# Kernel tuning notes

Measured on AMD Instinct MI355X. Metric: run time of the kernel, lower is better.

The kernel has to match this reference:

```python
import jax, jax.numpy as jnp
import numpy as np

C_M, C_Z, C, N_HEAD = 256, 128, 32, 8
N_SEQ, N_RES = 256, 256
LN_EPS = 1e-5


def _layer_norm(x, w, b):
    mu = jnp.mean(x, axis=-1, keepdims=True)
    var = jnp.var(x, axis=-1, keepdims=True)
    return (x - mu) * jax.lax.rsqrt(var + LN_EPS) * w + b


def setup_inputs() -> dict:
    key = jax.random.key(0)
    ks = jax.random.split(key, 12)
    s = 0.02
    return {
        "m": jax.random.normal(ks[0], (N_SEQ, N_RES, C_M), dtype=jnp.float32),
        "z": jax.random.normal(ks[1], (N_RES, N_RES, C_Z), dtype=jnp.float32),
        "ln_m_w": jnp.ones((C_M,), jnp.float32),
        "ln_m_b": jnp.zeros((C_M,), jnp.float32),
        "ln_z_w": jnp.ones((C_Z,), jnp.float32),
        "ln_z_b": jnp.zeros((C_Z,), jnp.float32),
        "Wz": jax.random.normal(ks[2], (C_Z, N_HEAD), dtype=jnp.float32) * s,
        "Wq": jax.random.normal(ks[3], (C_M, N_HEAD * C), dtype=jnp.float32) * s,
        "Wk": jax.random.normal(ks[4], (C_M, N_HEAD * C), dtype=jnp.float32) * s,
        "Wv": jax.random.normal(ks[5], (C_M, N_HEAD * C), dtype=jnp.float32) * s,
        "Wg": jax.random.normal(ks[6], (C_M, N_HEAD * C), dtype=jnp.float32) * s,
        "bg": jnp.zeros((N_HEAD * C,), jnp.float32),
        "Wo": jax.random.normal(ks[7], (N_HEAD * C, C_M), dtype=jnp.float32) * s,
        "bo": jnp.zeros((C_M,), jnp.float32),
    }


def reference(m, z, ln_m_w, ln_m_b, ln_z_w, ln_z_b, Wz, Wq, Wk, Wv, Wg, bg, Wo, bo):
    S, R, cm = m.shape
    mn = _layer_norm(m, ln_m_w, ln_m_b)            # (S, R, c_m)
    zn = _layer_norm(z, ln_z_w, ln_z_b)            # (R, R, c_z)
    bias = jnp.einsum('qkz,zh->hqk', zn, Wz)       # (H, R, R), pair bias per head

    Wqh = Wq.reshape(cm, N_HEAD, C)
    Wkh = Wk.reshape(cm, N_HEAD, C)
    Wvh = Wv.reshape(cm, N_HEAD, C)
    q = jnp.einsum('srm,mhc->shrc', mn, Wqh)       # (S, H, R, c)
    k = jnp.einsum('srm,mhc->shrc', mn, Wkh)
    v = jnp.einsum('srm,mhc->shrc', mn, Wvh)

    scale = 1.0 / jnp.sqrt(jnp.asarray(C, mn.dtype))
    scores = jnp.einsum('shqc,shkc->shqk', q, k) * scale + bias[None]  # (S, H, R, R)
    attn = jax.nn.softmax(scores, axis=-1)
    o = jnp.einsum('shqk,shkc->shqc', attn, v)     # (S, H, R, c)
    o = o.transpose(0, 2, 1, 3).reshape(S, R, N_HEAD * C)

    g = jax.nn.sigmoid(mn @ Wg + bg)               # gating, (S, R, H*c)
    return (g * o) @ Wo + bo                       # (S, R, c_m)
```

## Files before the change

### kernel.cpp

```cpp
#include <hip/hip_runtime.h>
#include <cmath>

#define NSEQ 256
#define NRES 256
#define CM   256
#define CZ   128
#define NHEAD 8
#define CHD  32
#define NROW 65536

typedef __attribute__((ext_vector_type(8))) short short8;
typedef __attribute__((ext_vector_type(4))) short s16x4;
typedef __attribute__((ext_vector_type(4))) float f32x4;

__device__ __forceinline__ unsigned short f2bf(float x) {
    union { float f; unsigned int u; } v; v.f = x;
    unsigned int u = v.u;
    u += 0x7fffu + ((u >> 16) & 1u);
    return (unsigned short)(u >> 16);
}
__device__ __forceinline__ float bf2f(unsigned short b) {
    union { float f; unsigned int u; } v; v.u = ((unsigned int)b) << 16;
    return v.f;
}

__device__ __forceinline__ void async16(const void* g, void* l) {
    __builtin_amdgcn_global_load_lds(
        (const __attribute__((address_space(1))) unsigned int*)g,
        (__attribute__((address_space(3))) unsigned int*)l, 16, 0, 0);
}

__device__ __forceinline__ void xcd_remap(int& x, int& y) {
    const int nx = gridDim.x, ny = gridDim.y;
    const int b = blockIdx.x + blockIdx.y * nx;
    if ((ny & 7) == 0) {
        const int c = b & 7;
        const int t = b >> 3;
        x = t % nx;
        y = c + 8 * (t / nx);
    } else {
        x = blockIdx.x; y = blockIdx.y;
    }
}

__global__ void __launch_bounds__(64)
ln_m_kernel(const float* __restrict__ m, const float* __restrict__ w,
            const float* __restrict__ b, unsigned short* __restrict__ mbf) {
    const int row = blockIdx.x;
    const int t = threadIdx.x;
    const float* x = m + (size_t)row * CM;
    float4 xv = *(const float4*)(x + t * 4);
    float s  = xv.x + xv.y + xv.z + xv.w;
    float s2 = xv.x * xv.x + xv.y * xv.y + xv.z * xv.z + xv.w * xv.w;
#pragma unroll
    for (int off = 32; off > 0; off >>= 1) {
        s  += __shfl_xor(s, off);
        s2 += __shfl_xor(s2, off);
    }
    const float mu  = s * (1.0f / CM);
    const float var = s2 * (1.0f / CM) - mu * mu;
    const float inv = rsqrtf(var + 1e-5f);
    float4 wv = *(const float4*)(w + t * 4);
    float4 bv = *(const float4*)(b + t * 4);
    ushort4 o4;
    o4.x = f2bf((xv.x - mu) * inv * wv.x + bv.x);
    o4.y = f2bf((xv.y - mu) * inv * wv.y + bv.y);
    o4.z = f2bf((xv.z - mu) * inv * wv.z + bv.z);
    o4.w = f2bf((xv.w - mu) * inv * wv.w + bv.w);
    *(ushort4*)(mbf + (size_t)row * CM + t * 4) = o4;
}

__global__ void __launch_bounds__(64)
ln_z_bias_kernel(const float* __restrict__ z, const float* __restrict__ w,
                 const float* __restrict__ b, const float* __restrict__ Wz,
                 float* __restrict__ bias) {
    const int pair = blockIdx.x;
    const int t = threadIdx.x;
    const float* x = z + (size_t)pair * CZ;
    float2 xv = *(const float2*)(x + t * 2);
    float s  = xv.x + xv.y;
    float s2 = xv.x * xv.x + xv.y * xv.y;
#pragma unroll
    for (int off = 32; off > 0; off >>= 1) {
        s  += __shfl_xor(s, off);
        s2 += __shfl_xor(s2, off);
    }
    const float mu  = s * (1.0f / CZ);
    const float var = s2 * (1.0f / CZ) - mu * mu;
    const float inv = rsqrtf(var + 1e-5f);
    float2 wv = *(const float2*)(w + t * 2);
    float2 bv = *(const float2*)(b + t * 2);
    const float zn0 = (xv.x - mu) * inv * wv.x + bv.x;
    const float zn1 = (xv.y - mu) * inv * wv.y + bv.y;
    float ph[NHEAD];
#pragma unroll
    for (int h = 0; h < NHEAD; h++)
        ph[h] = zn0 * Wz[(2 * t) * NHEAD + h] + zn1 * Wz[(2 * t + 1) * NHEAD + h];
#pragma unroll
    for (int h = 0; h < NHEAD; h++) {
#pragma unroll
        for (int off = 32; off > 0; off >>= 1) ph[h] += __shfl_xor(ph[h], off);
    }
    if (t == 0) {
#pragma unroll
        for (int h = 0; h < NHEAD; h++)
            bias[(size_t)h * NROW + pair] = ph[h];
    }
}

__global__ void __launch_bounds__(256)
bias_tr_kernel(const float* __restrict__ bq, float* __restrict__ bt) {
    __shared__ float tile[32][33];
    const int h = blockIdx.z;
    const int q0 = blockIdx.y * 32, k0 = blockIdx.x * 32;
    const int tr = threadIdx.x >> 5, tc = threadIdx.x & 31;
#pragma unroll
    for (int i = 0; i < 4; i++)
        tile[tr + i * 8][tc] = bq[(size_t)h * NROW + (size_t)(q0 + tr + i * 8) * 256 + k0 + tc];
    __syncthreads();
#pragma unroll
    for (int i = 0; i < 4; i++)
        bt[(size_t)h * NROW + (size_t)(k0 + tr + i * 8) * 256 + q0 + tc] = tile[tc][tr + i * 8];
}

__global__ void __launch_bounds__(256)
wsplit_kernel(const float* __restrict__ Wq, const float* __restrict__ Wk,
              const float* __restrict__ Wv, const float* __restrict__ Wg,
              const float* __restrict__ Wo, unsigned short* __restrict__ wbf) {
    const int n = blockIdx.x;
    const int mat = blockIdx.y;
    const int k = threadIdx.x;
    const float* W = (mat == 0) ? Wq : (mat == 1) ? Wk : (mat == 2) ? Wv
                   : (mat == 3) ? Wg : Wo;
    const float v = W[(size_t)k * 256 + n];
    unsigned short h = f2bf(v);
    unsigned short* hi = wbf + (size_t)mat * 65536;
    hi[(size_t)n * 256 + k] = h;
    if (mat == 4) {
        unsigned short* lo = wbf + (size_t)5 * 65536;
        lo[(size_t)n * 256 + k] = f2bf(v - bf2f(h));
    }
}

__device__ __forceinline__ void gemm128_1p(
    const unsigned short* __restrict__ A_g, const unsigned short* __restrict__ Bt_g,
    int m0, int n0, short* A_s, short* B_s,
    unsigned short* __restrict__ C, const float* __restrict__ bias,
    float alpha, int act) {
    const int tid  = threadIdx.x;
    const int wid  = tid >> 6;
    const int lane = tid & 63;
    const int wm = (wid >> 1) * 64;
    const int wn = (wid & 1) * 64;

    f32x4 acc[4][4];
#pragma unroll
    for (int i = 0; i < 4; i++)
#pragma unroll
        for (int j = 0; j < 4; j++) acc[i][j] = (f32x4){0.f, 0.f, 0.f, 0.f};

    const unsigned short* gmat = (wid < 2) ? A_g : Bt_g;
    short* lmat = (wid < 2) ? A_s : B_s;
    const int brow = (wid < 2) ? m0 : n0;
    const int half = (wid & 1) * 64;
    const int srow = lane >> 2;
    const int skq  = (lane & 3) * 8;

    const int lrow = lane & 15;
    const int lk   = (lane >> 4) * 8;

    for (int k0 = 0; k0 < 256; k0 += 32) {
#pragma unroll
        for (int r = 0; r < 4; r++) {
            const unsigned short* g = gmat + (size_t)(brow + half + r * 16 + srow) * 256 + k0 + skq;
            short* l = lmat + (half + r * 16) * 32;
            async16(g, l);
        }
        __syncthreads();

        short8 ah[4], bh[4];
#pragma unroll
        for (int f = 0; f < 4; f++) {
            ah[f] = *(const short8*)&A_s[(wm + f * 16 + lrow) * 32 + lk];
            bh[f] = *(const short8*)&B_s[(wn + f * 16 + lrow) * 32 + lk];
        }
#pragma unroll
        for (int i = 0; i < 4; i++)
#pragma unroll
            for (int j = 0; j < 4; j++)
                acc[i][j] = __builtin_amdgcn_mfma_f32_16x16x32_bf16(ah[i], bh[j], acc[i][j], 0, 0, 0);
        __syncthreads();
    }

    const int ccol0 = lane & 15;
    const int crow0 = (lane >> 4) * 4;
    float bvv[4];
#pragma unroll
    for (int j = 0; j < 4; j++)
        bvv[j] = bias ? bias[n0 + wn + j * 16 + ccol0] : 0.0f;
#pragma unroll
    for (int i = 0; i < 4; i++) {
#pragma unroll
        for (int r = 0; r < 4; r++) {
            const int row = m0 + wm + i * 16 + crow0 + r;
#pragma unroll
            for (int j = 0; j < 4; j++) {
                const int col = n0 + wn + j * 16 + ccol0;
                float v = acc[i][j][r] * alpha + bvv[j];
                if (act == 1) v = 1.0f / (1.0f + __expf(-v));
                C[(size_t)row * 256 + col] = f2bf(v);
            }
        }
    }
}

__global__ void __launch_bounds__(256)
gemm_qkvg_kernel(const unsigned short* __restrict__ A,
                 const unsigned short* __restrict__ wbf,
                 unsigned short* __restrict__ qb, unsigned short* __restrict__ kb,
                 unsigned short* __restrict__ vb, unsigned short* __restrict__ gb,
                 const float* __restrict__ bg, float scale) {
    __shared__ short A_s[128 * 32];
    __shared__ short B_s[128 * 32];
    int bx, by;
    xcd_remap(bx, by);
    const int which = bx >> 1;
    const int n0 = (bx & 1) * 128;
    const int m0 = by * 128;
    const unsigned short* bt = wbf + (size_t)which * 65536;
    unsigned short* C = (which == 0) ? qb : (which == 1) ? kb : (which == 2) ? vb : gb;
    const float alpha = (which == 0) ? scale : 1.0f;
    const float* bias = (which == 3) ? bg : nullptr;
    const int act = (which == 3) ? 1 : 0;
    gemm128_1p(A, bt, m0, n0, A_s, B_s, C, bias, alpha, act);
}

__global__ void __launch_bounds__(256)
gemm_out_kernel(const unsigned int* __restrict__ Ap_g,
                const unsigned short* __restrict__ wbf, float* __restrict__ C,
                const float* __restrict__ bo) {
    __shared__ unsigned int Ap_s[128 * 32];
    __shared__ short Bhi_s[128 * 32];
    __shared__ short Blo_s[128 * 32];
    int bx, by;
    xcd_remap(bx, by);
    const int m0 = by * 128, n0 = bx * 128;
    const unsigned short* Bthi_g = wbf + (size_t)4 * 65536;
    const unsigned short* Btlo_g = wbf + (size_t)5 * 65536;

    const int tid  = threadIdx.x;
    const int wid  = tid >> 6;
    const int lane = tid & 63;
    const int wm = (wid >> 1) * 64;
    const int wn = (wid & 1) * 64;

    f32x4 acc[4][4];
#pragma unroll
    for (int i = 0; i < 4; i++)
#pragma unroll
        for (int j = 0; j < 4; j++) acc[i][j] = (f32x4){0.f, 0.f, 0.f, 0.f};

    const int lrow = lane & 15;
    const int lk   = (lane >> 4) * 8;

    for (int k0 = 0; k0 < 256; k0 += 32) {
        if (wid < 2) {
            const int half = wid * 64;
            const int srow = lane >> 3;
            const int scol = (lane & 7) * 4;
#pragma unroll
            for (int r = 0; r < 8; r++) {
                const unsigned int* g = Ap_g + (size_t)(m0 + half + r * 8 + srow) * 256 + k0 + scol;
                unsigned int* l = Ap_s + (half + r * 8) * 32;
                async16(g, l);
            }
        } else {
            const unsigned short* gmat = (wid == 2) ? Bthi_g : Btlo_g;
            short* lmat = (wid == 2) ? Bhi_s : Blo_s;
            const int srow = lane >> 2;
            const int skq  = (lane & 3) * 8;
#pragma unroll
            for (int r = 0; r < 8; r++) {
                const unsigned short* g = gmat + (size_t)(n0 + r * 16 + srow) * 256 + k0 + skq;
                short* l = lmat + (r * 16) * 32;
                async16(g, l);
            }
        }
        __syncthreads();

        short8 ah[4], al[4], bh[4], bl[4];
#pragma unroll
        for (int f = 0; f < 4; f++) {
            const uint4* ap = (const uint4*)&Ap_s[(wm + f * 16 + lrow) * 32 + lk];
            uint4 a0 = ap[0], a1 = ap[1];
            union { unsigned int u[4]; short8 s; } uh, ul;
            uh.u[0] = __builtin_amdgcn_perm(a0.y, a0.x, 0x07060302u);
            uh.u[1] = __builtin_amdgcn_perm(a0.w, a0.z, 0x07060302u);
            uh.u[2] = __builtin_amdgcn_perm(a1.y, a1.x, 0x07060302u);
            uh.u[3] = __builtin_amdgcn_perm(a1.w, a1.z, 0x07060302u);
            ul.u[0] = __builtin_amdgcn_perm(a0.y, a0.x, 0x05040100u);
            ul.u[1] = __builtin_amdgcn_perm(a0.w, a0.z, 0x05040100u);
            ul.u[2] = __builtin_amdgcn_perm(a1.y, a1.x, 0x05040100u);
            ul.u[3] = __builtin_amdgcn_perm(a1.w, a1.z, 0x05040100u);
            ah[f] = uh.s; al[f] = ul.s;
            bh[f] = *(const short8*)&Bhi_s[(wn + f * 16 + lrow) * 32 + lk];
            bl[f] = *(const short8*)&Blo_s[(wn + f * 16 + lrow) * 32 + lk];
        }
#pragma unroll
        for (int i = 0; i < 4; i++)
#pragma unroll
            for (int j = 0; j < 4; j++) {
                acc[i][j] = __builtin_amdgcn_mfma_f32_16x16x32_bf16(ah[i], bh[j], acc[i][j], 0, 0, 0);
                acc[i][j] = __builtin_amdgcn_mfma_f32_16x16x32_bf16(ah[i], bl[j], acc[i][j], 0, 0, 0);
                acc[i][j] = __builtin_amdgcn_mfma_f32_16x16x32_bf16(al[i], bh[j], acc[i][j], 0, 0, 0);
            }
        __syncthreads();
    }

    const int ccol0 = lane & 15;
    const int crow0 = (lane >> 4) * 4;
    float bvv[4];
#pragma unroll
    for (int j = 0; j < 4; j++)
        bvv[j] = bo[n0 + wn + j * 16 + ccol0];
#pragma unroll
    for (int i = 0; i < 4; i++) {
#pragma unroll
        for (int r = 0; r < 4; r++) {
            const int row = m0 + wm + i * 16 + crow0 + r;
#pragma unroll
            for (int j = 0; j < 4; j++) {
                const int col = n0 + wn + j * 16 + ccol0;
                C[(size_t)row * 256 + col] = acc[i][j][r] + bvv[j];
            }
        }
    }
}

__global__ void __launch_bounds__(256, 4)
attn_mfma_kernel(const unsigned short* __restrict__ q, const unsigned short* __restrict__ k,
                 const unsigned short* __restrict__ v, const float* __restrict__ bias_t,
                 const unsigned short* __restrict__ g,
                 unsigned int* __restrict__ opack) {
    const int s = blockIdx.x, h = blockIdx.y;
    __shared__ short Ks[256][40];
    __shared__ short Vs[32][268];
    __shared__ float li_s[4][64];
    const int tid = threadIdx.x;
    const int w = tid >> 6, l = tid & 63;
    const int lg = l >> 4, l15 = l & 15;
    const size_t sbase = (size_t)s * (NRES * CM);

    {
        const int kk0 = tid >> 2;
        const int c8 = (tid & 3) * 8;
#pragma unroll
        for (int r4 = 0; r4 < 4; r4++) {
            const int kk = r4 * 64 + kk0;
            const size_t gi = sbase + (size_t)kk * CM + h * CHD + c8;
            short8 k8 = *(const short8*)(k + gi);
            short8 v8 = *(const short8*)(v + gi);
            *(short8*)&Ks[kk][c8] = k8;
#pragma unroll
            for (int jj = 0; jj < 8; jj++) Vs[c8 + jj][kk] = v8[jj];
        }
    }
    const int wq0 = w * 64;
    short8 qf[4];
#pragma unroll
    for (int mq = 0; mq < 4; mq++)
        qf[mq] = *(const short8*)(q + sbase + (size_t)(wq0 + mq * 16 + l15) * CM + h * CHD + lg * 8);
    __syncthreads();

    f32x4 acco[4][2];
#pragma unroll
    for (int mq = 0; mq < 4; mq++)
#pragma unroll
        for (int nc = 0; nc < 2; nc++) acco[mq][nc] = (f32x4){0.f, 0.f, 0.f, 0.f};
    float lip[4] = {0.f, 0.f, 0.f, 0.f};
    const float* bt = bias_t + (size_t)h * NROW;

    for (int ch = 0; ch < 8; ch++) {
        const int kb = ch * 32;
        short8 kf[2];
#pragma unroll
        for (int ik = 0; ik < 2; ik++)
            kf[ik] = *(const short8*)&Ks[kb + ik * 16 + l15][lg * 8];
#pragma unroll
        for (int ik = 0; ik < 2; ik++) {
            s16x4 vf[2];
#pragma unroll
            for (int nc = 0; nc < 2; nc++)
                vf[nc] = *(const s16x4*)&Vs[nc * 16 + l15][kb + ik * 16 + lg * 4];
            const int kk0a = kb + ik * 16 + lg * 4;
#pragma unroll
            for (int jq = 0; jq < 4; jq++) {
                const int qrow = wq0 + jq * 16 + l15;
                f32x4 sa = (f32x4){0.f, 0.f, 0.f, 0.f};
                sa = __builtin_amdgcn_mfma_f32_16x16x32_bf16(kf[ik], qf[jq], sa, 0, 0, 0);
                const float b0 = bt[(size_t)(kk0a + 0) * 256 + qrow];
                const float b1 = bt[(size_t)(kk0a + 1) * 256 + qrow];
                const float b2 = bt[(size_t)(kk0a + 2) * 256 + qrow];
                const float b3 = bt[(size_t)(kk0a + 3) * 256 + qrow];
                const float p0 = __expf(sa[0] + b0);
                const float p1 = __expf(sa[1] + b1);
                const float p2 = __expf(sa[2] + b2);
                const float p3 = __expf(sa[3] + b3);
                lip[jq] += (p0 + p1) + (p2 + p3);
                s16x4 pa;
                pa[0] = (short)f2bf(p0); pa[1] = (short)f2bf(p1);
                pa[2] = (short)f2bf(p2); pa[3] = (short)f2bf(p3);
#pragma unroll
                for (int nc = 0; nc < 2; nc++)
                    acco[jq][nc] = __builtin_amdgcn_mfma_f32_16x16x16bf16_1k(
                        pa, vf[nc], acco[jq][nc], 0, 0, 0);
            }
        }
    }

#pragma unroll
    for (int jq = 0; jq < 4; jq++) {
        lip[jq] += __shfl_xor(lip[jq], 16);
        lip[jq] += __shfl_xor(lip[jq], 32);
        li_s[w][jq * 16 + l15] = lip[jq];
    }

#pragma unroll
    for (int mq = 0; mq < 4; mq++) {
#pragma unroll
        for (int r = 0; r < 4; r++) {
            const int qrow = wq0 + mq * 16 + lg * 4 + r;
            const float inv = 1.0f / li_s[w][mq * 16 + lg * 4 + r];
            const size_t rb = sbase + (size_t)qrow * CM + h * CHD;
#pragma unroll
            for (int nc = 0; nc < 2; nc++) {
                const int c = nc * 16 + l15;
                const float val = acco[mq][nc][r] * inv * bf2f(g[rb + c]);
                const unsigned short hi = f2bf(val);
                const unsigned short lo = f2bf(val - bf2f(hi));
                opack[rb + c] = ((unsigned int)hi << 16) | lo;
            }
        }
    }
}

extern "C" void kernel_launch(void* const* d_in, const int* in_sizes, int n_in,
                              void* d_out, int out_size, void* d_ws, size_t ws_size,
                              hipStream_t stream) {
    const float* m    = (const float*)d_in[0];
    const float* z    = (const float*)d_in[1];
    const float* lnmw = (const float*)d_in[2];
    const float* lnmb = (const float*)d_in[3];
    const float* lnzw = (const float*)d_in[4];
    const float* lnzb = (const float*)d_in[5];
    const float* Wz   = (const float*)d_in[6];
    const float* Wq   = (const float*)d_in[7];
    const float* Wk   = (const float*)d_in[8];
    const float* Wv   = (const float*)d_in[9];
    const float* Wg   = (const float*)d_in[10];
    const float* bg   = (const float*)d_in[11];
    const float* Wo   = (const float*)d_in[12];
    const float* bo   = (const float*)d_in[13];
    float* out = (float*)d_out;

    char* wsb = (char*)d_ws;
    const size_t BIASB = (size_t)NHEAD * NROW * 4;
    const size_t WBFB  = (size_t)6 * 65536 * 2;
    float* bias_qk = (float*)wsb;
    float* bias_t  = (float*)(wsb + BIASB);
    unsigned short* wbf = (unsigned short*)(wsb + 2 * BIASB);
    char* chunk0 = wsb + 2 * BIASB + ((WBFB + 255) & ~(size_t)255);

    const size_t avail = ws_size - (size_t)(chunk0 - wsb);
    int SC = NSEQ;
    while (SC > 1 && (size_t)SC * NRES * CM * 14 > avail) SC >>= 1;
    const size_t CHE = (size_t)SC * NRES * CM;

    unsigned short* qb  = (unsigned short*)chunk0;
    unsigned short* kb  = qb + CHE;
    unsigned short* vb  = kb + CHE;
    unsigned short* gb  = vb + CHE;
    unsigned short* mbf = gb + CHE;
    unsigned int* opk   = (unsigned int*)(mbf + CHE);

    ln_z_bias_kernel<<<NROW, 64, 0, stream>>>(z, lnzw, lnzb, Wz, bias_qk);
    bias_tr_kernel<<<dim3(8, 8, 8), 256, 0, stream>>>(bias_qk, bias_t);
    wsplit_kernel<<<dim3(256, 5), 256, 0, stream>>>(Wq, Wk, Wv, Wg, Wo, wbf);

    const int rows = SC * NRES;
    const int mtiles = rows / 128;
    const float scale = 0.17677669529663687f;

    for (int s0 = 0; s0 < NSEQ; s0 += SC) {
        const float* m_c   = m   + (size_t)s0 * NRES * CM;
        float*       out_c = out + (size_t)s0 * NRES * CM;

        ln_m_kernel<<<rows, 64, 0, stream>>>(m_c, lnmw, lnmb, mbf);

        gemm_qkvg_kernel<<<dim3(8, mtiles), 256, 0, stream>>>(
            mbf, wbf, qb, kb, vb, gb, bg, scale);

        attn_mfma_kernel<<<dim3(SC, NHEAD), 256, 0, stream>>>(
            qb, kb, vb, bias_t, gb, opk);

        gemm_out_kernel<<<dim3(2, mtiles), 256, 0, stream>>>(
            opk, wbf, out_c, bo);
    }
}
```

Before: 399.1 us.

## Use head-major Q/K/V/G layout, drop bias transpose, fold log2e into exp2

Q, K, V, G and the packed output are now stored head-major ([head][row][32]) so each attention block reads a contiguous slab per head. The pair-bias transpose kernel is removed and attention reads the untransposed bias as one float4 per MFMA fragment instead of four strided scalar loads. Bias and Q scale are premultiplied by log2(e) so the softmax can use the hardware exp2 directly. The QKVG GEMM epilogue now writes scattered 32-column chunks, which may cost some store efficiency.

```diff
diff --git a/kernel.cpp b/kernel.cpp
--- a/kernel.cpp
+++ b/kernel.cpp
@@ -104,23 +104,8 @@
     if (t == 0) {
 #pragma unroll
         for (int h = 0; h < NHEAD; h++)
-            bias[(size_t)h * NROW + pair] = ph[h];
-    }
-}
-
-__global__ void __launch_bounds__(256)
-bias_tr_kernel(const float* __restrict__ bq, float* __restrict__ bt) {
-    __shared__ float tile[32][33];
-    const int h = blockIdx.z;
-    const int q0 = blockIdx.y * 32, k0 = blockIdx.x * 32;
-    const int tr = threadIdx.x >> 5, tc = threadIdx.x & 31;
-#pragma unroll
-    for (int i = 0; i < 4; i++)
-        tile[tr + i * 8][tc] = bq[(size_t)h * NROW + (size_t)(q0 + tr + i * 8) * 256 + k0 + tc];
-    __syncthreads();
-#pragma unroll
-    for (int i = 0; i < 4; i++)
-        bt[(size_t)h * NROW + (size_t)(k0 + tr + i * 8) * 256 + q0 + tc] = tile[tc][tr + i * 8];
+            bias[(size_t)h * NROW + pair] = ph[h] * 1.4426950408889634f;
+    }
 }
 
 __global__ void __launch_bounds__(256)
@@ -144,7 +129,7 @@
 
 __device__ __forceinline__ void gemm128_1p(
     const unsigned short* __restrict__ A_g, const unsigned short* __restrict__ Bt_g,
-    int m0, int n0, short* A_s, short* B_s,
+    int m0, int n0, int rowsTot, short* A_s, short* B_s,
     unsigned short* __restrict__ C, const float* __restrict__ bias,
     float alpha, int act) {
     const int tid  = threadIdx.x;
@@ -208,7 +193,7 @@
                 const int col = n0 + wn + j * 16 + ccol0;
                 float v = acc[i][j][r] * alpha + bvv[j];
                 if (act == 1) v = 1.0f / (1.0f + __expf(-v));
-                C[(size_t)row * 256 + col] = f2bf(v);
+                C[((size_t)(col >> 5) * rowsTot + row) * 32 + (col & 31)] = f2bf(v);
             }
         }
     }
@@ -219,7 +204,7 @@
                  const unsigned short* __restrict__ wbf,
                  unsigned short* __restrict__ qb, unsigned short* __restrict__ kb,
                  unsigned short* __restrict__ vb, unsigned short* __restrict__ gb,
-                 const float* __restrict__ bg, float scale) {
+                 const float* __restrict__ bg, float scale, int rowsTot) {
     __shared__ short A_s[128 * 32];
     __shared__ short B_s[128 * 32];
     int bx, by;
@@ -232,13 +217,13 @@
     const float alpha = (which == 0) ? scale : 1.0f;
     const float* bias = (which == 3) ? bg : nullptr;
     const int act = (which == 3) ? 1 : 0;
-    gemm128_1p(A, bt, m0, n0, A_s, B_s, C, bias, alpha, act);
+    gemm128_1p(A, bt, m0, n0, rowsTot, A_s, B_s, C, bias, alpha, act);
 }
 
 __global__ void __launch_bounds__(256)
 gemm_out_kernel(const unsigned int* __restrict__ Ap_g,
                 const unsigned short* __restrict__ wbf, float* __restrict__ C,
-                const float* __restrict__ bo) {
+                const float* __restrict__ bo, int rowsTot) {
     __shared__ unsigned int Ap_s[128 * 32];
     __shared__ short Bhi_s[128 * 32];
     __shared__ short Blo_s[128 * 32];
@@ -270,7 +255,8 @@
             const int scol = (lane & 7) * 4;
 #pragma unroll
             for (int r = 0; r < 8; r++) {
-                const unsigned int* g = Ap_g + (size_t)(m0 + half + r * 8 + srow) * 256 + k0 + scol;
+                const unsigned int* g = Ap_g
+                    + ((size_t)(k0 >> 5) * rowsTot + m0 + half + r * 8 + srow) * 32 + scol;
                 unsigned int* l = Ap_s + (half + r * 8) * 32;
                 async16(g, l);
             }
@@ -339,9 +325,9 @@
 
 __global__ void __launch_bounds__(256, 4)
 attn_mfma_kernel(const unsigned short* __restrict__ q, const unsigned short* __restrict__ k,
-                 const unsigned short* __restrict__ v, const float* __restrict__ bias_t,
+                 const unsigned short* __restrict__ v, const float* __restrict__ bias_qk,
                  const unsigned short* __restrict__ g,
-                 unsigned int* __restrict__ opack) {
+                 unsigned int* __restrict__ opack, int rows) {
     const int s = blockIdx.x, h = blockIdx.y;
     __shared__ short Ks[256][40];
     __shared__ short Vs[32][268];
@@ -349,7 +335,7 @@
     const int tid = threadIdx.x;
     const int w = tid >> 6, l = tid & 63;
     const int lg = l >> 4, l15 = l & 15;
-    const size_t sbase = (size_t)s * (NRES * CM);
+    const size_t hb = ((size_t)h * rows + (size_t)s * NRES) * 32;
 
     {
         const int kk0 = tid >> 2;
@@ -357,7 +343,7 @@
 #pragma unroll
         for (int r4 = 0; r4 < 4; r4++) {
             const int kk = r4 * 64 + kk0;
-            const size_t gi = sbase + (size_t)kk * CM + h * CHD + c8;
+            const size_t gi = hb + (size_t)kk * 32 + c8;
             short8 k8 = *(const short8*)(k + gi);
             short8 v8 = *(const short8*)(v + gi);
             *(short8*)&Ks[kk][c8] = k8;
@@ -369,7 +355,7 @@
     short8 qf[4];
 #pragma unroll
     for (int mq = 0; mq < 4; mq++)
-        qf[mq] = *(const short8*)(q + sbase + (size_t)(wq0 + mq * 16 + l15) * CM + h * CHD + lg * 8);
+        qf[mq] = *(const short8*)(q + hb + (size_t)(wq0 + mq * 16 + l15) * 32 + lg * 8);
     __syncthreads();
 
     f32x4 acco[4][2];
@@ -378,7 +364,7 @@
 #pragma unroll
         for (int nc = 0; nc < 2; nc++) acco[mq][nc] = (f32x4){0.f, 0.f, 0.f, 0.f};
     float lip[4] = {0.f, 0.f, 0.f, 0.f};
-    const float* bt = bias_t + (size_t)h * NROW;
+    const float* bh = bias_qk + (size_t)h * NROW;
 
     for (int ch = 0; ch < 8; ch++) {
         const int kb = ch * 32;
@@ -392,20 +378,17 @@
 #pragma unroll
             for (int nc = 0; nc < 2; nc++)
                 vf[nc] = *(const s16x4*)&Vs[nc * 16 + l15][kb + ik * 16 + lg * 4];
-            const int kk0a = kb + ik * 16 + lg * 4;
+            const int kkr = ik * 16 + lg * 4;
 #pragma unroll
             for (int jq = 0; jq < 4; jq++) {
                 const int qrow = wq0 + jq * 16 + l15;
                 f32x4 sa = (f32x4){0.f, 0.f, 0.f, 0.f};
                 sa = __builtin_amdgcn_mfma_f32_16x16x32_bf16(kf[ik], qf[jq], sa, 0, 0, 0);
-                const float b0 = bt[(size_t)(kk0a + 0) * 256 + qrow];
-                const float b1 = bt[(size_t)(kk0a + 1) * 256 + qrow];
-                const float b2 = bt[(size_t)(kk0a + 2) * 256 + qrow];
-                const float b3 = bt[(size_t)(kk0a + 3) * 256 + qrow];
-                const float p0 = __expf(sa[0] + b0);
-                const float p1 = __expf(sa[1] + b1);
-                const float p2 = __expf(sa[2] + b2);
-                const float p3 = __expf(sa[3] + b3);
+                float4 bv = *(const float4*)(bh + (size_t)qrow * NRES + kb + kkr);
+                const float p0 = __builtin_amdgcn_exp2f(sa[0] + bv.x);
+                const float p1 = __builtin_amdgcn_exp2f(sa[1] + bv.y);
+                const float p2 = __builtin_amdgcn_exp2f(sa[2] + bv.z);
+                const float p3 = __builtin_amdgcn_exp2f(sa[3] + bv.w);
                 lip[jq] += (p0 + p1) + (p2 + p3);
                 s16x4 pa;
                 pa[0] = (short)f2bf(p0); pa[1] = (short)f2bf(p1);
@@ -431,7 +414,7 @@
         for (int r = 0; r < 4; r++) {
             const int qrow = wq0 + mq * 16 + lg * 4 + r;
             const float inv = 1.0f / li_s[w][mq * 16 + lg * 4 + r];
-            const size_t rb = sbase + (size_t)qrow * CM + h * CHD;
+            const size_t rb = hb + (size_t)qrow * 32;
 #pragma unroll
             for (int nc = 0; nc < 2; nc++) {
                 const int c = nc * 16 + l15;
@@ -467,9 +450,8 @@
     const size_t BIASB = (size_t)NHEAD * NROW * 4;
     const size_t WBFB  = (size_t)6 * 65536 * 2;
     float* bias_qk = (float*)wsb;
-    float* bias_t  = (float*)(wsb + BIASB);
-    unsigned short* wbf = (unsigned short*)(wsb + 2 * BIASB);
-    char* chunk0 = wsb + 2 * BIASB + ((WBFB + 255) & ~(size_t)255);
+    unsigned short* wbf = (unsigned short*)(wsb + BIASB);
+    char* chunk0 = wsb + BIASB + ((WBFB + 255) & ~(size_t)255);
 
     const size_t avail = ws_size - (size_t)(chunk0 - wsb);
     int SC = NSEQ;
@@ -484,12 +466,11 @@
     unsigned int* opk   = (unsigned int*)(mbf + CHE);
 
     ln_z_bias_kernel<<<NROW, 64, 0, stream>>>(z, lnzw, lnzb, Wz, bias_qk);
-    bias_tr_kernel<<<dim3(8, 8, 8), 256, 0, stream>>>(bias_qk, bias_t);
     wsplit_kernel<<<dim3(256, 5), 256, 0, stream>>>(Wq, Wk, Wv, Wg, Wo, wbf);
 
     const int rows = SC * NRES;
     const int mtiles = rows / 128;
-    const float scale = 0.17677669529663687f;
+    const float scale = 0.17677669529663687f * 1.4426950408889634f;
 
     for (int s0 = 0; s0 < NSEQ; s0 += SC) {
         const float* m_c   = m   + (size_t)s0 * NRES * CM;
@@ -498,12 +479,12 @@
         ln_m_kernel<<<rows, 64, 0, stream>>>(m_c, lnmw, lnmb, mbf);
 
         gemm_qkvg_kernel<<<dim3(8, mtiles), 256, 0, stream>>>(
-            mbf, wbf, qb, kb, vb, gb, bg, scale);
+            mbf, wbf, qb, kb, vb, gb, bg, scale, rows);
 
         attn_mfma_kernel<<<dim3(SC, NHEAD), 256, 0, stream>>>(
-            qb, kb, vb, bias_t, gb, opk);
+            qb, kb, vb, bias_qk, gb, opk, rows);
 
         gemm_out_kernel<<<dim3(2, mtiles), 256, 0, stream>>>(
-            opk, wbf, out_c, bo);
-    }
-}
+            opk, wbf, out_c, bo, rows);
+    }
+}
```

After: 373.1 us. 1.07x faster.
